# Optimization experiments

Measured on AMD Instinct MI355X. Metric: run time of the kernel, lower is better.

The kernel has to match this reference:

```python
import jax, jax.numpy as jnp
import numpy as np
from jax import lax

N, D, M, H = 8192, 32, 8, 128
ATOL = 1e-5
RTOL = 1e-5
MAX_STEPS = 10   # bounded adaptive dopri5 iterations (accept/reject with masking)
DT0 = 0.25


def setup_inputs() -> dict:
    key = jax.random.key(0)
    ks = jax.random.split(key, 6)
    p = lambda k, shape, s: jax.random.normal(k, shape, jnp.float32) * s
    return {
        "z": jax.random.normal(ks[0], (N, D), jnp.float32),
        "G_w": p(ks[1], (M, D), 0.3),
        "W1": p(ks[2], (H, D), (1.0 / D) ** 0.5),
        "b1": jnp.zeros((H,), jnp.float32),
        "W2": p(ks[3], (H, H), (1.0 / H) ** 0.5),
        "b2": jnp.zeros((H,), jnp.float32),
        "W3": p(ks[4], (D, H), (1.0 / H) ** 0.5),
        "b3": jnp.zeros((D,), jnp.float32),
        "T": jnp.ones((1,), jnp.float32),
    }


def qpnf_forward(z, G_w, W1, b1, W2, b2, W3, b3, T):
    d = z.shape[1]

    def mlp(x):  # dF network: d -> 128 -> 128 -> d
        h = jax.nn.relu(x @ W1.T + b1)
        h = jax.nn.relu(h @ W2.T + b2)
        return h @ W3.T + b3

    # G is linear (no bias) so jacrev(G)(x) == G_w for every sample; the batched
    # dG @ dG^T solves collapse to one shared (m,m) solve / (d,d) projector.
    A = G_w @ G_w.T                       # (m, m)
    AinvG = jnp.linalg.solve(A, G_w)      # (m, d) = A^{-1} W
    P = G_w.T @ AinvG                     # (d, d) null-space projector W^T A^{-1} W
    IP = jnp.eye(d, dtype=z.dtype) - P
    trP = jnp.trace(P)

    jac_mlp = jax.vmap(jax.jacrev(lambda xi: mlp(xi[None, :])[0]))  # (N,d,d)

    def f(y):  # augmented state y = [x | logp], dlogp/dt = -div(dx/dx)
        x = y[:, :d]
        dF = mlp(x)                        # (N, d)
        g = x @ G_w.T                      # (N, m)
        dz = -(dF @ IP) - g @ AinvG        # -(eta_J) - (eta_C)
        JdF = jac_mlp(x)                   # (N, d, d)
        # J_f = -(I-P) JdF - P  ->  dlogp = -trace(J_f)
        dlogp = jnp.einsum('jk,nkj->n', IP, JdF) + trP
        return jnp.concatenate([dz, dlogp[:, None]], axis=1)

    def rk_step(y, dt):  # Dormand-Prince 5(4)
        k1 = f(y)
        k2 = f(y + dt * (0.2 * k1))
        k3 = f(y + dt * (3/40 * k1 + 9/40 * k2))
        k4 = f(y + dt * (44/45 * k1 - 56/15 * k2 + 32/9 * k3))
        k5 = f(y + dt * (19372/6561 * k1 - 25360/2187 * k2 + 64448/6561 * k3 - 212/729 * k4))
        k6 = f(y + dt * (9017/3168 * k1 - 355/33 * k2 + 46732/5247 * k3 + 49/176 * k4 - 5103/18656 * k5))
        y1 = y + dt * (35/384 * k1 + 500/1113 * k3 + 125/192 * k4 - 2187/6784 * k5 + 11/84 * k6)
        k7 = f(y1)
        err = dt * ((35/384 - 5179/57600) * k1 + (500/1113 - 7571/16695) * k3
                    + (125/192 - 393/640) * k4 + (-2187/6784 + 92097/339200) * k5
                    + (11/84 - 187/2100) * k6 - (1/40) * k7)
        return y1, err

    t1 = 2.0 * T[0]  # eval path: integration_times[-1] *= 2
    y0 = jnp.concatenate([z, jnp.zeros((z.shape[0], 1), z.dtype)], axis=1)

    def body(carry, _):
        t, dt, y = carry
        done = t >= t1 - 1e-9
        dtc = jnp.where(done, jnp.asarray(1e-3, z.dtype), jnp.minimum(dt, t1 - t))
        y1, ev = rk_step(y, dtc)
        tol = ATOL + RTOL * jnp.maximum(jnp.abs(y), jnp.abs(y1))
        errn = jnp.sqrt(jnp.mean((ev / tol) ** 2))
        accept = jnp.logical_and(~done, errn <= 1.0)
        y_new = jnp.where(accept, y1, y)
        t_new = jnp.where(accept, t + dtc, t)
        factor = jnp.clip(0.9 * errn ** (-0.2), 0.2, 10.0)
        dt_new = jnp.where(done, dt, jnp.clip(dtc * factor, 1e-6, t1))
        dt_new = lax.stop_gradient(dt_new)
        return (t_new, dt_new, y_new), None

    init = (jnp.asarray(0.0, z.dtype), jnp.asarray(DT0, z.dtype), y0)
    (_, _, yT), _ = lax.scan(body, init, None, length=MAX_STEPS)
    return yT[:, :d]


def reference(z, G_w, W1, b1, W2, b2, W3, b3, T):
    return qpnf_forward(z, G_w, W1, b1, W2, b2, W3, b3, T)
```

## Files before the change

kernel.cpp:

```cpp
#include <hip/hip_runtime.h>
#include <hip/hip_cooperative_groups.h>
#include <math.h>

namespace cg = cooperative_groups;
typedef float4 f4;

#define NT 512
#define RB 32

#define WS_WR    0
#define WS_PART  32768
#define WS_YZ    35328
#define WS_Y1Z   297472
#define WS_YL    559616
#define WS_Y1L   567808
#define WS_KZ    576000
#define WS_KL    2411008
#define WS_TOTAL 2468352

#define L_W1T   0
#define L_C3T   4096
#define L_P     8320
#define L_PT    9344
#define L_HST   10496
#define L_HS2   15104
#define L_XST   19712
#define L_B1    20864
#define L_B2    20992
#define L_C0    21120
#define L_GS    21152
#define L_AAUG  21408
#define L_AINVG 21536
#define L_MISC  21792
#define LDS_FLOATS 21793
#define L_RED   L_XST

__device__ const float ACO[5][5] = {
  { 0.2f, 0.f, 0.f, 0.f, 0.f },
  { (float)(3.0/40.0), (float)(9.0/40.0), 0.f, 0.f, 0.f },
  { (float)(44.0/45.0), (float)(-56.0/15.0), (float)(32.0/9.0), 0.f, 0.f },
  { (float)(19372.0/6561.0), (float)(-25360.0/2187.0), (float)(64448.0/6561.0), (float)(-212.0/729.0), 0.f },
  { (float)(9017.0/3168.0), (float)(-355.0/33.0), (float)(46732.0/5247.0), (float)(49.0/176.0), (float)(-5103.0/18656.0) }
};

#define B1C ((float)(35.0/384.0))
#define B3C ((float)(500.0/1113.0))
#define B4C ((float)(125.0/192.0))
#define B5C ((float)(-2187.0/6784.0))
#define B6C ((float)(11.0/84.0))

#define E1C ((float)(35.0/384.0 - 5179.0/57600.0))
#define E3C ((float)(500.0/1113.0 - 7571.0/16695.0))
#define E4C ((float)(125.0/192.0 - 393.0/640.0))
#define E5C ((float)(-2187.0/6784.0 + 92097.0/339200.0))
#define E6C ((float)(11.0/84.0 - 187.0/2100.0))
#define E7C ((float)(-1.0/40.0))

__device__ __forceinline__ f4 ld4(const float* p){ return *(const f4*)p; }
__device__ __forceinline__ void st4(float* p, f4 v){ *(f4*)p = v; }

__device__ void assemble_x(float* lds, const float* __restrict__ ws, int r0, int tid,
                           float dtc, const float* co, int np)
{
  __syncthreads();
  if (tid < 256){
    const int r = tid >> 3, jj = (tid & 7) * 4;
    const int base = (r0 + r) * 32 + jj;
    f4 y = ld4(&ws[WS_YZ + base]);
    float sx = 0.f, sy = 0.f, sz = 0.f, sw = 0.f;
    for (int p = 0; p < np; p++){
      f4 kv = ld4(&ws[WS_KZ + p * 262144 + base]);
      float c = co[p];
      sx += c * kv.x; sy += c * kv.y; sz += c * kv.z; sw += c * kv.w;
    }
    lds[L_XST + (jj + 0) * 36 + r] = y.x + dtc * sx;
    lds[L_XST + (jj + 1) * 36 + r] = y.y + dtc * sy;
    lds[L_XST + (jj + 2) * 36 + r] = y.z + dtc * sz;
    lds[L_XST + (jj + 3) * 36 + r] = y.w + dtc * sw;
  }
  __syncthreads();
}

__device__ void eval_f(float* lds, float* __restrict__ ws, int r0, int tid,
                       float trP, int kout)
{
  const int cg = tid & 31, kh = (tid >> 5) & 1, wv = tid >> 6;
  const int row4 = 4 * wv;

  float a1[4][4];
#pragma unroll
  for (int i = 0; i < 4; i++)
#pragma unroll
    for (int j = 0; j < 4; j++) a1[i][j] = 0.f;
#pragma unroll 4
  for (int t = 0; t < 16; t++){
    const int k = kh * 16 + t;
    f4 av = ld4(&lds[L_XST + k * 36 + row4]);
    f4 bv = ld4(&lds[L_W1T + k * 128 + 4 * cg]);
    const float* ap = (const float*)&av;
    const float* bp = (const float*)&bv;
#pragma unroll
    for (int i = 0; i < 4; i++)
#pragma unroll
      for (int j = 0; j < 4; j++) a1[i][j] += bp[i] * ap[j];
  }
#pragma unroll
  for (int i = 0; i < 4; i++)
#pragma unroll
    for (int j = 0; j < 4; j++) a1[i][j] += __shfl_xor(a1[i][j], 32);
  if (kh == 0){
    f4 b1v = ld4(&lds[L_B1 + 4 * cg]);
    const float* b1p = (const float*)&b1v;
#pragma unroll
    for (int i = 0; i < 4; i++){
      f4 hv; float* hp = (float*)&hv;
#pragma unroll
      for (int j = 0; j < 4; j++) hp[j] = fmaxf(a1[i][j] + b1p[i], 0.f);
      st4(&lds[L_HST + (4 * cg + i) * 36 + row4], hv);
    }
  }
  __syncthreads();

  float ah[4][4], at[4][4];
#pragma unroll
  for (int i = 0; i < 4; i++)
#pragma unroll
    for (int j = 0; j < 4; j++){ ah[i][j] = 0.f; at[i][j] = 0.f; }
  const f4* WR4 = (const f4*)&ws[WS_WR];
  const int kb = kh * 64;
  f4 wb[4], rb[4];
#pragma unroll
  for (int u = 0; u < 4; u++){
    wb[u] = WR4[(kb + u) * 64 + cg];
    rb[u] = WR4[(kb + u) * 64 + 32 + cg];
  }
#pragma unroll 1
  for (int g = 0; g < 16; g++){
    f4 wc[4], rc[4];
#pragma unroll
    for (int u = 0; u < 4; u++){ wc[u] = wb[u]; rc[u] = rb[u]; }
    if (g < 15){
      const int kn = kb + (g + 1) * 4;
#pragma unroll
      for (int u = 0; u < 4; u++){
        wb[u] = WR4[(kn + u) * 64 + cg];
        rb[u] = WR4[(kn + u) * 64 + 32 + cg];
      }
    }
#pragma unroll
    for (int u = 0; u < 4; u++){
      const int k = kb + g * 4 + u;
      f4 av = ld4(&lds[L_HST + k * 36 + row4]);
      const float* ap = (const float*)&av;
      const float* wp = (const float*)&wc[u];
      const float* rp = (const float*)&rc[u];
      float m[4];
#pragma unroll
      for (int j = 0; j < 4; j++) m[j] = (ap[j] > 0.f) ? 1.f : 0.f;
#pragma unroll
      for (int i = 0; i < 4; i++)
#pragma unroll
        for (int j = 0; j < 4; j++){
          ah[i][j] += wp[i] * ap[j];
          at[i][j] += rp[i] * m[j];
        }
    }
  }
#pragma unroll
  for (int i = 0; i < 4; i++)
#pragma unroll
    for (int j = 0; j < 4; j++){
      ah[i][j] += __shfl_xor(ah[i][j], 32);
      at[i][j] += __shfl_xor(at[i][j], 32);
    }

  f4 b2v = ld4(&lds[L_B2 + 4 * cg]);
  const float* b2p = (const float*)&b2v;
  float h2v[4][4]; float dl[4] = {0.f, 0.f, 0.f, 0.f};
#pragma unroll
  for (int i = 0; i < 4; i++)
#pragma unroll
    for (int j = 0; j < 4; j++){
      float pre = ah[i][j] + b2p[i];
      float hv = fmaxf(pre, 0.f);
      h2v[i][j] = hv;
      if (pre > 0.f) dl[j] += at[i][j];
    }
#pragma unroll
  for (int mk = 1; mk < 32; mk <<= 1){
#pragma unroll
    for (int j = 0; j < 4; j++) dl[j] += __shfl_xor(dl[j], mk, 64);
  }
  if (kh == 0){
#pragma unroll
    for (int i = 0; i < 4; i++){
      f4 hv; float* hp = (float*)&hv;
#pragma unroll
      for (int j = 0; j < 4; j++) hp[j] = h2v[i][j];
      st4(&lds[L_HS2 + (4 * cg + i) * 36 + row4], hv);
    }
    if (cg == 0){
#pragma unroll
      for (int j = 0; j < 4; j++)
        ws[WS_KL + kout * 8192 + r0 + row4 + j] = dl[j] + trP;
    }
  }
  __syncthreads();

  float a3[4] = {0.f, 0.f, 0.f, 0.f};
  const int bb = kh * 64;
#pragma unroll 4
  for (int t = 0; t < 16; t++){
    f4 cv = ld4(&lds[L_C3T + cg * 132 + bb + 4 * t]);
    const float* cp = (const float*)&cv;
#pragma unroll
    for (int u = 0; u < 4; u++){
      f4 av = ld4(&lds[L_HS2 + (bb + 4 * t + u) * 36 + row4]);
      const float* ap = (const float*)&av;
#pragma unroll
      for (int j = 0; j < 4; j++) a3[j] += ap[j] * cp[u];
    }
  }
  const int qq = kh * 16;
#pragma unroll
  for (int t = 0; t < 4; t++){
    f4 pv = ld4(&lds[L_PT + cg * 36 + qq + 4 * t]);
    const float* pp = (const float*)&pv;
#pragma unroll
    for (int u = 0; u < 4; u++){
      f4 av = ld4(&lds[L_XST + (qq + 4 * t + u) * 36 + row4]);
      const float* ap = (const float*)&av;
#pragma unroll
      for (int j = 0; j < 4; j++) a3[j] += ap[j] * pp[u];
    }
  }
#pragma unroll
  for (int j = 0; j < 4; j++) a3[j] += __shfl_xor(a3[j], 32);
  if (kh == 0){
    float c0v = lds[L_C0 + cg];
#pragma unroll
    for (int j = 0; j < 4; j++)
      ws[WS_KZ + kout * 262144 + (r0 + row4 + j) * 32 + cg] = -(a3[j] + c0v);
  }
}

__global__ void __launch_bounds__(NT, 2)
qpnf_kernel(const float* __restrict__ z, const float* __restrict__ Gw,
            const float* __restrict__ W1g, const float* __restrict__ b1g,
            const float* __restrict__ W2g, const float* __restrict__ b2g,
            const float* __restrict__ W3g, const float* __restrict__ b3g,
            const float* __restrict__ Tg, float* __restrict__ out,
            float* __restrict__ ws)
{
  __shared__ float lds[LDS_FLOATS];
  const int tid = threadIdx.x;
  const int bid = blockIdx.x;
  const int r0 = bid * RB;
  cg::grid_group grid = cg::this_grid();

  for (int i = 0; i < 8; i++){
    int idx = tid + i * NT;
    int h = idx >> 5, j = idx & 31;
    lds[L_W1T + j * 128 + h] = W1g[idx];
  }
  if (tid < 128){ lds[L_B1 + tid] = b1g[tid]; lds[L_B2 + tid] = b2g[tid]; }
  if (tid < 256) lds[L_GS + tid] = Gw[tid];
  __syncthreads();

  if (tid < 64){
    int i = tid >> 3, j = tid & 7;
    float s = 0.f;
    for (int k = 0; k < 32; k++) s += lds[L_GS + i * 32 + k] * lds[L_GS + j * 32 + k];
    lds[L_AAUG + i * 16 + j] = s;
    lds[L_AAUG + i * 16 + 8 + j] = (i == j) ? 1.f : 0.f;
  }
  __syncthreads();
  if (tid == 0){
    float* A = &lds[L_AAUG];
    for (int c = 0; c < 8; c++){
      int p = c; float mx = fabsf(A[c * 16 + c]);
      for (int r = c + 1; r < 8; r++){
        float v = fabsf(A[r * 16 + c]);
        if (v > mx){ mx = v; p = r; }
      }
      if (p != c)
        for (int q = 0; q < 16; q++){ float t = A[c*16+q]; A[c*16+q] = A[p*16+q]; A[p*16+q] = t; }
      float pv = 1.0f / A[c * 16 + c];
      for (int q = 0; q < 16; q++) A[c * 16 + q] *= pv;
      for (int r = 0; r < 8; r++) if (r != c){
        float fct = A[r * 16 + c];
        for (int q = 0; q < 16; q++) A[r * 16 + q] -= fct * A[c * 16 + q];
      }
    }
  }
  __syncthreads();
  if (tid < 256){
    int m = tid >> 5, d = tid & 31;
    float s = 0.f;
    for (int q = 0; q < 8; q++) s += lds[L_AAUG + m * 16 + 8 + q] * lds[L_GS + q * 32 + d];
    lds[L_AINVG + m * 32 + d] = s;
  }
  __syncthreads();
  for (int i4 = 0; i4 < 2; i4++){
    int idx = tid + i4 * NT;
    int i = idx >> 5, j = idx & 31;
    float s = 0.f;
    for (int m = 0; m < 8; m++) s += lds[L_GS + m * 32 + i] * lds[L_AINVG + m * 32 + j];
    lds[L_P + i * 32 + j] = s;
  }
  __syncthreads();
  float* IPl = &lds[L_XST];
  for (int i4 = 0; i4 < 2; i4++){
    int idx = tid + i4 * NT;
    int i = idx >> 5, j = idx & 31;
    IPl[i * 32 + j] = ((i == j) ? 1.f : 0.f) - lds[L_P + i * 32 + j];
  }
  if (tid == 0){
    float s = 0.f;
    for (int i = 0; i < 32; i++) s += lds[L_P + i * 32 + i];
    lds[L_MISC] = s;
  }
  __syncthreads();
  for (int i4 = 0; i4 < 8; i4++){
    int idx = tid + i4 * NT;
    int b = idx & 127, c = idx >> 7;
    float s = 0.f;
    for (int i = 0; i < 32; i++) s += W3g[i * 128 + b] * IPl[i * 32 + c];
    lds[L_C3T + c * 132 + b] = s;
  }
  for (int i4 = 0; i4 < 2; i4++){
    int idx = tid + i4 * NT;
    int c = idx >> 5, q = idx & 31;
    lds[L_PT + c * 36 + q] = lds[L_P + q * 32 + c];
  }
  if (tid < 32){
    float s = 0.f;
    for (int i = 0; i < 32; i++) s += b3g[i] * IPl[i * 32 + tid];
    lds[L_C0 + tid] = s;
  }
  for (int i4 = 0; i4 < 8; i4++){
    int idx = tid + i4 * NT;
    int j = idx >> 7, b = idx & 127;
    float s = 0.f;
    for (int k = 0; k < 32; k++) s += IPl[j * 32 + k] * W3g[k * 128 + b];
    lds[L_HST + j * 128 + b] = s;
  }
  __syncthreads();
  if (bid < 128 && tid < 128){
    int a = bid;
    float s = 0.f;
    for (int j = 0; j < 32; j++) s += W1g[a * 32 + j] * lds[L_HST + j * 128 + tid];
    ws[WS_WR + a * 256 + 128 + tid] = s * W2g[tid * 128 + a];
  }
  if (bid >= 128 && tid < 128){
    int a = bid - 128;
    ws[WS_WR + a * 256 + tid] = W2g[tid * 128 + a];
  }
  if (tid < 256){
    const int r = tid >> 3, jj = (tid & 7) * 4;
    const int base = (r0 + r) * 32 + jj;
    st4(&ws[WS_YZ + base], ld4(&z[base]));
  }
  if (tid < RB) ws[WS_YL + r0 + tid] = 0.f;

  const float trP = lds[L_MISC];
  const float t1 = 2.0f * Tg[0];

  grid.sync();

  float t_cur = 0.f, dt_cur = 0.25f;
  bool prev_acc = false;

  for (int step = 0; step < 10; step++){
    if (t_cur >= t1 - 1e-9f) break;
    const float dtc = fminf(dt_cur, t1 - t_cur);

    for (int s = 1; s <= 6; s++){
      if (s == 1 && step > 0){
        if (prev_acc){
          if (tid < 256){
            const int r = tid >> 3, jj = (tid & 7) * 4;
            const int base = (r0 + r) * 32 + jj;
            st4(&ws[WS_KZ + 0 * 262144 + base], ld4(&ws[WS_KZ + 6 * 262144 + base]));
          }
          if (tid < RB) ws[WS_KL + 0 * 8192 + r0 + tid] = ws[WS_KL + 6 * 8192 + r0 + tid];
        }
        continue;
      }
      assemble_x(lds, ws, r0, tid, dtc, ACO[s >= 2 ? s - 2 : 0], s - 1);
      eval_f(lds, ws, r0, tid, trP, s - 1);
    }

    __syncthreads();
    if (tid < 256){
      const int r = tid >> 3, jj = (tid & 7) * 4;
      const int base = (r0 + r) * 32 + jj;
      f4 y   = ld4(&ws[WS_YZ + base]);
      f4 k1v = ld4(&ws[WS_KZ + 0 * 262144 + base]);
      f4 k3v = ld4(&ws[WS_KZ + 2 * 262144 + base]);
      f4 k4v = ld4(&ws[WS_KZ + 3 * 262144 + base]);
      f4 k5v = ld4(&ws[WS_KZ + 4 * 262144 + base]);
      f4 k6v = ld4(&ws[WS_KZ + 5 * 262144 + base]);
      f4 x;
      x.x = y.x + dtc * (B1C*k1v.x + B3C*k3v.x + B4C*k4v.x + B5C*k5v.x + B6C*k6v.x);
      x.y = y.y + dtc * (B1C*k1v.y + B3C*k3v.y + B4C*k4v.y + B5C*k5v.y + B6C*k6v.y);
      x.z = y.z + dtc * (B1C*k1v.z + B3C*k3v.z + B4C*k4v.z + B5C*k5v.z + B6C*k6v.z);
      x.w = y.w + dtc * (B1C*k1v.w + B3C*k3v.w + B4C*k4v.w + B5C*k5v.w + B6C*k6v.w);
      st4(&ws[WS_Y1Z + base], x);
      lds[L_XST + (jj + 0) * 36 + r] = x.x;
      lds[L_XST + (jj + 1) * 36 + r] = x.y;
      lds[L_XST + (jj + 2) * 36 + r] = x.z;
      lds[L_XST + (jj + 3) * 36 + r] = x.w;
    }
    if (tid < RB){
      int n = r0 + tid;
      float s = B1C * ws[WS_KL + 0*8192 + n] + B3C * ws[WS_KL + 2*8192 + n]
              + B4C * ws[WS_KL + 3*8192 + n] + B5C * ws[WS_KL + 4*8192 + n]
              + B6C * ws[WS_KL + 5*8192 + n];
      ws[WS_Y1L + n] = ws[WS_YL + n] + dtc * s;
    }
    __syncthreads();
    eval_f(lds, ws, r0, tid, trP, 6);
    __syncthreads();

    float sacc = 0.f;
    if (tid < 256){
      const int r = tid >> 3, jj = (tid & 7) * 4;
      const int base = (r0 + r) * 32 + jj;
      f4 k1v = ld4(&ws[WS_KZ + 0 * 262144 + base]);
      f4 k3v = ld4(&ws[WS_KZ + 2 * 262144 + base]);
      f4 k4v = ld4(&ws[WS_KZ + 3 * 262144 + base]);
      f4 k5v = ld4(&ws[WS_KZ + 4 * 262144 + base]);
      f4 k6v = ld4(&ws[WS_KZ + 5 * 262144 + base]);
      f4 k7v = ld4(&ws[WS_KZ + 6 * 262144 + base]);
      f4 yv  = ld4(&ws[WS_YZ + base]);
      f4 y1v = ld4(&ws[WS_Y1Z + base]);
      float ev, tol, q;
      ev = dtc * (E1C*k1v.x + E3C*k3v.x + E4C*k4v.x + E5C*k5v.x + E6C*k6v.x + E7C*k7v.x);
      tol = 1e-5f + 1e-5f * fmaxf(fabsf(yv.x), fabsf(y1v.x)); q = ev / tol; sacc += q * q;
      ev = dtc * (E1C*k1v.y + E3C*k3v.y + E4C*k4v.y + E5C*k5v.y + E6C*k6v.y + E7C*k7v.y);
      tol = 1e-5f + 1e-5f * fmaxf(fabsf(yv.y), fabsf(y1v.y)); q = ev / tol; sacc += q * q;
      ev = dtc * (E1C*k1v.z + E3C*k3v.z + E4C*k4v.z + E5C*k5v.z + E6C*k6v.z + E7C*k7v.z);
      tol = 1e-5f + 1e-5f * fmaxf(fabsf(yv.z), fabsf(y1v.z)); q = ev / tol; sacc += q * q;
      ev = dtc * (E1C*k1v.w + E3C*k3v.w + E4C*k4v.w + E5C*k5v.w + E6C*k6v.w + E7C*k7v.w);
      tol = 1e-5f + 1e-5f * fmaxf(fabsf(yv.w), fabsf(y1v.w)); q = ev / tol; sacc += q * q;
    }
    if (tid < RB){
      int n = r0 + tid;
      float evl = dtc * (E1C * ws[WS_KL + 0*8192 + n] + E3C * ws[WS_KL + 2*8192 + n]
                + E4C * ws[WS_KL + 3*8192 + n] + E5C * ws[WS_KL + 4*8192 + n]
                + E6C * ws[WS_KL + 5*8192 + n] + E7C * ws[WS_KL + 6*8192 + n]);
      float toll = 1e-5f + 1e-5f * fmaxf(fabsf(ws[WS_YL + n]), fabsf(ws[WS_Y1L + n]));
      float ql = evl / toll; sacc += ql * ql;
    }
    lds[L_RED + tid] = sacc; __syncthreads();
    for (int o = 256; o > 0; o >>= 1){
      if (tid < o) lds[L_RED + tid] += lds[L_RED + tid + o];
      __syncthreads();
    }
    if (tid == 0) ws[WS_PART + step * 256 + bid] = lds[L_RED + 0];

    grid.sync();

    if (tid < 256) lds[L_RED + tid] = ws[WS_PART + step * 256 + tid];
    __syncthreads();
    for (int o = 128; o > 0; o >>= 1){
      if (tid < o) lds[L_RED + tid] += lds[L_RED + tid + o];
      __syncthreads();
    }
    const float errn = sqrtf(lds[L_RED + 0] / 270336.0f);
    __syncthreads();

    const bool accept = (errn <= 1.0f);
    if (accept){
      if (tid < 256){
        const int r = tid >> 3, jj = (tid & 7) * 4;
        const int base = (r0 + r) * 32 + jj;
        st4(&ws[WS_YZ + base], ld4(&ws[WS_Y1Z + base]));
      }
      if (tid < RB) ws[WS_YL + r0 + tid] = ws[WS_Y1L + r0 + tid];
      t_cur += dtc;
    }
    float fac = 0.9f * powf(errn, -0.2f);
    fac = fminf(fmaxf(fac, 0.2f), 10.0f);
    dt_cur = fminf(fmaxf(dtc * fac, 1e-6f), t1);
    prev_acc = accept;
  }

  if (tid < 256){
    const int r = tid >> 3, jj = (tid & 7) * 4;
    const int base = (r0 + r) * 32 + jj;
    st4(&out[base], ld4(&ws[WS_YZ + base]));
  }
}

extern "C" void kernel_launch(void* const* d_in, const int* in_sizes, int n_in,
                              void* d_out, int out_size, void* d_ws, size_t ws_size,
                              hipStream_t stream)
{
  (void)in_sizes; (void)n_in; (void)out_size;
  const float* z  = (const float*)d_in[0];
  const float* Gw = (const float*)d_in[1];
  const float* W1 = (const float*)d_in[2];
  const float* b1 = (const float*)d_in[3];
  const float* W2 = (const float*)d_in[4];
  const float* b2 = (const float*)d_in[5];
  const float* W3 = (const float*)d_in[6];
  const float* b3 = (const float*)d_in[7];
  const float* T  = (const float*)d_in[8];
  float* out = (float*)d_out;
  float* ws  = (float*)d_ws;
  if (ws_size < (size_t)WS_TOTAL * sizeof(float)) return;

  void* args[] = { (void*)&z, (void*)&Gw, (void*)&W1, (void*)&b1, (void*)&W2,
                   (void*)&b2, (void*)&W3, (void*)&b3, (void*)&T, (void*)&out,
                   (void*)&ws };
  hipLaunchCooperativeKernel((const void*)qpnf_kernel, dim3(256), dim3(NT),
                             args, 0, stream);
}
```

Measured before the change: 1.360 ms.

## Keep per-block RK stage state and solution vectors in LDS instead of global workspace

Moves the per-row state (y, y1, logp parts and all seven RK stage vectors) from the global workspace into shared memory, padded to a stride of 36. Each block owns its 32 rows, so these values never need to be visible across blocks. This removes global memory round trips in every stage assembly, final combine and error estimate. LDS use per block grows from about 85KB to about 127KB, which may limit the two-blocks-per-CU occupancy set by the launch bounds and the cooperative grid's residency.

After: 1.300 ms. 4.4% less time.

```diff
diff --git a/kernel.cpp b/kernel.cpp
--- a/kernel.cpp
+++ b/kernel.cpp
@@ -10,13 +10,7 @@
 
 #define WS_WR    0
 #define WS_PART  32768
-#define WS_YZ    35328
-#define WS_Y1Z   297472
-#define WS_YL    559616
-#define WS_Y1L   567808
-#define WS_KZ    576000
-#define WS_KL    2411008
-#define WS_TOTAL 2468352
+#define WS_TOTAL 35328
 
 #define L_W1T   0
 #define L_C3T   4096
@@ -32,7 +26,13 @@
 #define L_AAUG  21408
 #define L_AINVG 21536
 #define L_MISC  21792
-#define LDS_FLOATS 21793
+#define L_KZ    21796
+#define L_KL    29860
+#define L_YZ    30084
+#define L_Y1Z   31236
+#define L_YL    32388
+#define L_Y1L   32420
+#define LDS_FLOATS 32452
 #define L_RED   L_XST
 
 __device__ const float ACO[5][5] = {
@@ -59,17 +59,16 @@
 __device__ __forceinline__ f4 ld4(const float* p){ return *(const f4*)p; }
 __device__ __forceinline__ void st4(float* p, f4 v){ *(f4*)p = v; }
 
-__device__ void assemble_x(float* lds, const float* __restrict__ ws, int r0, int tid,
-                           float dtc, const float* co, int np)
+__device__ void assemble_x(float* lds, int tid, float dtc, const float* co, int np)
 {
   __syncthreads();
   if (tid < 256){
     const int r = tid >> 3, jj = (tid & 7) * 4;
-    const int base = (r0 + r) * 32 + jj;
-    f4 y = ld4(&ws[WS_YZ + base]);
+    const int o = r * 36 + jj;
+    f4 y = ld4(&lds[L_YZ + o]);
     float sx = 0.f, sy = 0.f, sz = 0.f, sw = 0.f;
     for (int p = 0; p < np; p++){
-      f4 kv = ld4(&ws[WS_KZ + p * 262144 + base]);
+      f4 kv = ld4(&lds[L_KZ + p * 1152 + o]);
       float c = co[p];
       sx += c * kv.x; sy += c * kv.y; sz += c * kv.z; sw += c * kv.w;
     }
@@ -81,7 +80,7 @@
   __syncthreads();
 }
 
-__device__ void eval_f(float* lds, float* __restrict__ ws, int r0, int tid,
+__device__ void eval_f(float* lds, const float* __restrict__ ws, int tid,
                        float trP, int kout)
 {
   const int cg = tid & 31, kh = (tid >> 5) & 1, wv = tid >> 6;
@@ -202,7 +201,7 @@
     if (cg == 0){
 #pragma unroll
       for (int j = 0; j < 4; j++)
-        ws[WS_KL + kout * 8192 + r0 + row4 + j] = dl[j] + trP;
+        lds[L_KL + kout * 32 + row4 + j] = dl[j] + trP;
     }
   }
   __syncthreads();
@@ -240,7 +239,7 @@
     float c0v = lds[L_C0 + cg];
 #pragma unroll
     for (int j = 0; j < 4; j++)
-      ws[WS_KZ + kout * 262144 + (r0 + row4 + j) * 32 + cg] = -(a3[j] + c0v);
+      lds[L_KZ + kout * 1152 + (row4 + j) * 36 + cg] = -(a3[j] + c0v);
   }
 }
 
@@ -358,10 +357,9 @@
   }
   if (tid < 256){
     const int r = tid >> 3, jj = (tid & 7) * 4;
-    const int base = (r0 + r) * 32 + jj;
-    st4(&ws[WS_YZ + base], ld4(&z[base]));
-  }
-  if (tid < RB) ws[WS_YL + r0 + tid] = 0.f;
+    st4(&lds[L_YZ + r * 36 + jj], ld4(&z[(r0 + r) * 32 + jj]));
+  }
+  if (tid < RB) lds[L_YL + tid] = 0.f;
 
   const float trP = lds[L_MISC];
   const float t1 = 2.0f * Tg[0];
@@ -380,61 +378,60 @@
         if (prev_acc){
           if (tid < 256){
             const int r = tid >> 3, jj = (tid & 7) * 4;
-            const int base = (r0 + r) * 32 + jj;
-            st4(&ws[WS_KZ + 0 * 262144 + base], ld4(&ws[WS_KZ + 6 * 262144 + base]));
+            const int o = r * 36 + jj;
+            st4(&lds[L_KZ + o], ld4(&lds[L_KZ + 6 * 1152 + o]));
           }
-          if (tid < RB) ws[WS_KL + 0 * 8192 + r0 + tid] = ws[WS_KL + 6 * 8192 + r0 + tid];
+          if (tid < RB) lds[L_KL + tid] = lds[L_KL + 6 * 32 + tid];
         }
         continue;
       }
-      assemble_x(lds, ws, r0, tid, dtc, ACO[s >= 2 ? s - 2 : 0], s - 1);
-      eval_f(lds, ws, r0, tid, trP, s - 1);
+      assemble_x(lds, tid, dtc, ACO[s >= 2 ? s - 2 : 0], s - 1);
+      eval_f(lds, ws, tid, trP, s - 1);
     }
 
     __syncthreads();
     if (tid < 256){
       const int r = tid >> 3, jj = (tid & 7) * 4;
-      const int base = (r0 + r) * 32 + jj;
-      f4 y   = ld4(&ws[WS_YZ + base]);
-      f4 k1v = ld4(&ws[WS_KZ + 0 * 262144 + base]);
-      f4 k3v = ld4(&ws[WS_KZ + 2 * 262144 + base]);
-      f4 k4v = ld4(&ws[WS_KZ + 3 * 262144 + base]);
-      f4 k5v = ld4(&ws[WS_KZ + 4 * 262144 + base]);
-      f4 k6v = ld4(&ws[WS_KZ + 5 * 262144 + base]);
+      const int o = r * 36 + jj;
+      f4 y   = ld4(&lds[L_YZ + o]);
+      f4 k1v = ld4(&lds[L_KZ + 0 * 1152 + o]);
+      f4 k3v = ld4(&lds[L_KZ + 2 * 1152 + o]);
+      f4 k4v = ld4(&lds[L_KZ + 3 * 1152 + o]);
+      f4 k5v = ld4(&lds[L_KZ + 4 * 1152 + o]);
+      f4 k6v = ld4(&lds[L_KZ + 5 * 1152 + o]);
       f4 x;
       x.x = y.x + dtc * (B1C*k1v.x + B3C*k3v.x + B4C*k4v.x + B5C*k5v.x + B6C*k6v.x);
       x.y = y.y + dtc * (B1C*k1v.y + B3C*k3v.y + B4C*k4v.y + B5C*k5v.y + B6C*k6v.y);
       x.z = y.z + dtc * (B1C*k1v.z + B3C*k3v.z + B4C*k4v.z + B5C*k5v.z + B6C*k6v.z);
       x.w = y.w + dtc * (B1C*k1v.w + B3C*k3v.w + B4C*k4v.w + B5C*k5v.w + B6C*k6v.w);
-      st4(&ws[WS_Y1Z + base], x);
+      st4(&lds[L_Y1Z + o], x);
       lds[L_XST + (jj + 0) * 36 + r] = x.x;
       lds[L_XST + (jj + 1) * 36 + r] = x.y;
       lds[L_XST + (jj + 2) * 36 + r] = x.z;
       lds[L_XST + (jj + 3) * 36 + r] = x.w;
     }
     if (tid < RB){
-      int n = r0 + tid;
-      float s = B1C * ws[WS_KL + 0*8192 + n] + B3C * ws[WS_KL + 2*8192 + n]
-              + B4C * ws[WS_KL + 3*8192 + n] + B5C * ws[WS_KL + 4*8192 + n]
-              + B6C * ws[WS_KL + 5*8192 + n];
-      ws[WS_Y1L + n] = ws[WS_YL + n] + dtc * s;
+      float s = B1C * lds[L_KL + 0*32 + tid] + B3C * lds[L_KL + 2*32 + tid]
+              + B4C * lds[L_KL + 3*32 + tid] + B5C * lds[L_KL + 4*32 + tid]
+              + B6C * lds[L_KL + 5*32 + tid];
+      lds[L_Y1L + tid] = lds[L_YL + tid] + dtc * s;
     }
     __syncthreads();
-    eval_f(lds, ws, r0, tid, trP, 6);
+    eval_f(lds, ws, tid, trP, 6);
     __syncthreads();
 
     float sacc = 0.f;
     if (tid < 256){
       const int r = tid >> 3, jj = (tid & 7) * 4;
-      const int base = (r0 + r) * 32 + jj;
-      f4 k1v = ld4(&ws[WS_KZ + 0 * 262144 + base]);
-      f4 k3v = ld4(&ws[WS_KZ + 2 * 262144 + base]);
-      f4 k4v = ld4(&ws[WS_KZ + 3 * 262144 + base]);
-      f4 k5v = ld4(&ws[WS_KZ + 4 * 262144 + base]);
-      f4 k6v = ld4(&ws[WS_KZ + 5 * 262144 + base]);
-      f4 k7v = ld4(&ws[WS_KZ + 6 * 262144 + base]);
-      f4 yv  = ld4(&ws[WS_YZ + base]);
-      f4 y1v = ld4(&ws[WS_Y1Z + base]);
+      const int o = r * 36 + jj;
+      f4 k1v = ld4(&lds[L_KZ + 0 * 1152 + o]);
+      f4 k3v = ld4(&lds[L_KZ + 2 * 1152 + o]);
+      f4 k4v = ld4(&lds[L_KZ + 3 * 1152 + o]);
+      f4 k5v = ld4(&lds[L_KZ + 4 * 1152 + o]);
+      f4 k6v = ld4(&lds[L_KZ + 5 * 1152 + o]);
+      f4 k7v = ld4(&lds[L_KZ + 6 * 1152 + o]);
+      f4 yv  = ld4(&lds[L_YZ + o]);
+      f4 y1v = ld4(&lds[L_Y1Z + o]);
       float ev, tol, q;
       ev = dtc * (E1C*k1v.x + E3C*k3v.x + E4C*k4v.x + E5C*k5v.x + E6C*k6v.x + E7C*k7v.x);
       tol = 1e-5f + 1e-5f * fmaxf(fabsf(yv.x), fabsf(y1v.x)); q = ev / tol; sacc += q * q;
@@ -446,13 +443,13 @@
       tol = 1e-5f + 1e-5f * fmaxf(fabsf(yv.w), fabsf(y1v.w)); q = ev / tol; sacc += q * q;
     }
     if (tid < RB){
-      int n = r0 + tid;
-      float evl = dtc * (E1C * ws[WS_KL + 0*8192 + n] + E3C * ws[WS_KL + 2*8192 + n]
-                + E4C * ws[WS_KL + 3*8192 + n] + E5C * ws[WS_KL + 4*8192 + n]
-                + E6C * ws[WS_KL + 5*8192 + n] + E7C * ws[WS_KL + 6*8192 + n]);
-      float toll = 1e-5f + 1e-5f * fmaxf(fabsf(ws[WS_YL + n]), fabsf(ws[WS_Y1L + n]));
+      float evl = dtc * (E1C * lds[L_KL + 0*32 + tid] + E3C * lds[L_KL + 2*32 + tid]
+                + E4C * lds[L_KL + 3*32 + tid] + E5C * lds[L_KL + 4*32 + tid]
+                + E6C * lds[L_KL + 5*32 + tid] + E7C * lds[L_KL + 6*32 + tid]);
+      float toll = 1e-5f + 1e-5f * fmaxf(fabsf(lds[L_YL + tid]), fabsf(lds[L_Y1L + tid]));
       float ql = evl / toll; sacc += ql * ql;
     }
+    __syncthreads();
     lds[L_RED + tid] = sacc; __syncthreads();
     for (int o = 256; o > 0; o >>= 1){
       if (tid < o) lds[L_RED + tid] += lds[L_RED + tid + o];
@@ -475,10 +472,10 @@
     if (accept){
       if (tid < 256){
         const int r = tid >> 3, jj = (tid & 7) * 4;
-        const int base = (r0 + r) * 32 + jj;
-        st4(&ws[WS_YZ + base], ld4(&ws[WS_Y1Z + base]));
+        const int o = r * 36 + jj;
+        st4(&lds[L_YZ + o], ld4(&lds[L_Y1Z + o]));
       }
-      if (tid < RB) ws[WS_YL + r0 + tid] = ws[WS_Y1L + r0 + tid];
+      if (tid < RB) lds[L_YL + tid] = lds[L_Y1L + tid];
       t_cur += dtc;
     }
     float fac = 0.9f * powf(errn, -0.2f);
@@ -487,10 +484,10 @@
     prev_acc = accept;
   }
 
+  __syncthreads();
   if (tid < 256){
     const int r = tid >> 3, jj = (tid & 7) * 4;
-    const int base = (r0 + r) * 32 + jj;
-    st4(&out[base], ld4(&ws[WS_YZ + base]));
+    st4(&out[(r0 + r) * 32 + jj], ld4(&lds[L_YZ + r * 36 + jj]));
   }
 }
 
```
